# Optimization experiments

Measured on AMD Instinct MI355X. Metric: run time of the kernel, lower is better.

The kernel has to match this reference:

```python
import jax, jax.numpy as jnp
import numpy as np
from jax import lax

K = 7  # kernel_size
PAD = K // 2


def _feature_difference(t):
    # t: [B, C, H, W] -> normalized census-style local differences [B, K*K, H, W]
    intensity = t.mean(axis=1, keepdims=True)  # [B,1,H,W]
    # Equivalent to conv2d with the identity (eye) kernel in the torch module:
    # channel k gathers the neighbor at offset (k//K, k%K) with zero padding.
    patches = lax.conv_general_dilated_patches(
        intensity, filter_shape=(K, K), window_strides=(1, 1),
        padding=[(PAD, PAD), (PAD, PAD)])  # [B, K*K, H, W]
    local_diff = patches - intensity
    return local_diff / jnp.sqrt(0.81 + local_diff * local_diff)


def setup_inputs() -> dict:
    key = jax.random.key(0)
    kx, ky = jax.random.split(key)
    B, C, H, W = 8, 3, 320, 1024
    x = jax.random.uniform(kx, (B, C, H, W), dtype=jnp.float32)
    y = jax.random.uniform(ky, (B, C, H, W), dtype=jnp.float32)
    return {"x": x, "y": y}


def reference(x, y):
    diff_x = _feature_difference(x)
    diff_y = _feature_difference(y)
    diff_total = diff_x - lax.stop_gradient(diff_y)  # .detach() on y branch
    d2 = diff_total * diff_total
    dist = (d2 / (0.1 + d2)).mean(axis=1, keepdims=True)  # [B,1,H,W]
    b, c, h, w = x.shape
    # valid-region mask: ones in the interior, zeros in the PAD-wide border
    mask = jnp.zeros((b, 1, h, w), dtype=x.dtype)
    mask = mask.at[:, :, PAD:h - PAD, PAD:w - PAD].set(1.0)
    return (dist * mask).mean()
```

## Files before the change

kernel.cpp:

```cpp
#include <hip/hip_runtime.h>

typedef float f32x2 __attribute__((ext_vector_type(2)));
typedef float f32x4 __attribute__((ext_vector_type(4)));

#define PAD 3
#define HH 320
#define WW 1024
#define BB 8
#define TH 32
#define TW 64
#define HALO_H (TH + 2*PAD)
#define LDS_W  72
#define NF4    (LDS_W/4)
#define NPOS   (HALO_H * NF4)
#define RPW 4
#define NWAVES 8
#define NTHREADS (NWAVES * 64)

#define NIN ((HH - 2*PAD) * (WW - 2*PAD))
#define OUT_SCALE (1.0 / (49.0 * (double)BB * (double)HH * (double)WW))
#define C0 ((float)(48.0 * (double)BB * (double)NIN * OUT_SCALE))
#define NEG_SCALE ((float)(-0.1 * OUT_SCALE))

#define KEEP(v) asm("" : "+v"(v))

__device__ __forceinline__ f32x2 mk2(float a, float b) { f32x2 r; r.x = a; r.y = b; return r; }
__device__ __forceinline__ f32x2 sp2(float a)          { f32x2 r; r.x = a; r.y = a; return r; }
__device__ __forceinline__ f32x2 fma2(f32x2 a, f32x2 b, f32x2 c) {
    return __builtin_elementwise_fma(a, b, c);
}

template<bool INTERIOR>
__device__ __forceinline__ void pair2(f32x2 nx, f32x2 ny, f32x2 cx2, f32x2 cy2,
                                      f32x2 w2, float& acc)
{
    f32x2 dx  = nx - cx2;
    f32x2 dy  = ny - cy2;
    f32x2 dx2 = dx * dx;
    f32x2 dy2 = dy * dy;
    f32x2 ax  = dx2 + sp2(0.81f);
    f32x2 ay  = dy2 + sp2(0.81f);
    f32x2 P   = ax * ay;
    f32x2 s   = mk2(__builtin_amdgcn_rsqf(P.x), __builtin_amdgcn_rsqf(P.y));
    f32x2 A   = fma2(dx2, ay, dy2 * ax);
    f32x2 h   = dx * dy;
    f32x2 inner = fma2(s, A, h * sp2(-2.0f));
    f32x2 t2  = s * inner;
    f32x2 den = t2 + sp2(0.1f);
    float ip    = __builtin_amdgcn_rcpf(den.x * den.y);
    float cross;
    if constexpr (INTERIOR) cross = den.x + den.y;
    else                    cross = fmaf(w2.x, den.y, w2.y * den.x);
    acc = fmaf(ip, cross, acc);
}

template<bool INTERIOR>
__device__ __forceinline__ float compute_rows(
    const float (&sIx)[HALO_H][LDS_W], const float (&sIy)[HALO_H][LDS_W],
    int tile_i, int tile_j, int tx, int wv)
{
    float cO[7] = {};
    f32x2 cP0 = {}, cP1 = {}, cP2 = {}, cP3 = {};
    if constexpr (!INTERIOR) {
        const int gj = tile_j + tx;
        #pragma unroll
        for (int d = 0; d < 7; ++d) {
            int nj = gj + d - 3;
            cO[d] = (nj >= PAD && nj < WW - PAD) ? 1.0f : 0.0f;
        }
        cP0 = mk2(cO[0], cO[1]);
        cP1 = mk2(cO[2], cO[3]);
        cP2 = mk2(cO[4], cO[5]);
        cP3 = sp2(cO[6]);
    }

    const int li0 = wv * RPW;

    float wx[4][7], wy[4][7];
    #pragma unroll
    for (int r = 0; r < 3; ++r) {
        #pragma unroll
        for (int d = 0; d < 7; ++d) {
            float a = sIx[li0 + 3 + r][tx + 1 + d]; KEEP(a); wx[r][d] = a;
            float c = sIy[li0 + 3 + r][tx + 1 + d]; KEEP(c); wy[r][d] = c;
        }
    }

    float acc = 0.0f;

    #pragma unroll
    for (int iu = 0; iu < RPW; ++iu) {
        const int li = li0 + iu;
        const int gi = tile_i + li;
        const int snew = (iu + 3) & 3;
        #pragma unroll
        for (int d = 0; d < 7; ++d) {
            float a = sIx[li + 6][tx + 1 + d]; KEEP(a); wx[snew][d] = a;
            float c = sIy[li + 6][tx + 1 + d]; KEEP(c); wy[snew][d] = c;
        }

        float rin[4] = {};
        f32x2 mc2 = {};
        if constexpr (!INTERIOR) {
            #pragma unroll
            for (int di = 0; di < 4; ++di) {
                int ni = gi + di;
                rin[di] = (ni >= PAD && ni < HH - PAD) ? 1.0f : 0.0f;
            }
            mc2 = sp2(rin[0] * cO[3]);
        }

        const int s0 = iu & 3;
        const f32x2 cx2 = sp2(wx[s0][3]);
        const f32x2 cy2 = sp2(wy[s0][3]);

        pair2<INTERIOR>(mk2(wx[s0][4], wx[s0][5]), mk2(wy[s0][4], wy[s0][5]),
              cx2, cy2, INTERIOR ? sp2(0.0f) : fma2(sp2(rin[0]), cP2, mc2), acc);

        #pragma unroll
        for (int di = 1; di <= 3; ++di) {
            const int s = (iu + di) & 3;
            const f32x2 rin2 = sp2(rin[di]);
            pair2<INTERIOR>(mk2(wx[s][0], wx[s][1]), mk2(wy[s][0], wy[s][1]),
                  cx2, cy2, INTERIOR ? sp2(0.0f) : fma2(rin2, cP0, mc2), acc);
            pair2<INTERIOR>(mk2(wx[s][2], wx[s][3]), mk2(wy[s][2], wy[s][3]),
                  cx2, cy2, INTERIOR ? sp2(0.0f) : fma2(rin2, cP1, mc2), acc);
            pair2<INTERIOR>(mk2(wx[s][4], wx[s][5]), mk2(wy[s][4], wy[s][5]),
                  cx2, cy2, INTERIOR ? sp2(0.0f) : fma2(rin2, cP2, mc2), acc);
        }

        {
            const int s1 = (iu + 1) & 3;
            const int s2 = (iu + 2) & 3;
            const int s3 = (iu + 3) & 3;
            pair2<INTERIOR>(mk2(wx[s0][6], wx[s1][6]), mk2(wy[s0][6], wy[s1][6]),
                  cx2, cy2, INTERIOR ? sp2(0.0f) : fma2(mk2(rin[0], rin[1]), cP3, mc2), acc);
            pair2<INTERIOR>(mk2(wx[s2][6], wx[s3][6]), mk2(wy[s2][6], wy[s3][6]),
                  cx2, cy2, INTERIOR ? sp2(0.0f) : fma2(mk2(rin[2], rin[3]), cP3, mc2), acc);
        }
    }

    return acc;
}

__global__ __launch_bounds__(NTHREADS, 4) void ternary_loss_kernel(
    const float* __restrict__ x, const float* __restrict__ y,
    float* __restrict__ out)
{
    __shared__ __align__(16) float sIx[HALO_H][LDS_W];
    __shared__ __align__(16) float sIy[HALO_H][LDS_W];
    __shared__ float wave_sums[NWAVES];

    const int tile_j = blockIdx.x * TW;
    const int tile_i = blockIdx.y * TH;
    const int b      = blockIdx.z;
    const int tx  = threadIdx.x;
    const int wv  = threadIdx.y;
    const int tid = wv * 64 + tx;

    const size_t PLANE = (size_t)HH * WW;
    const float* xb = x + (size_t)b * 3 * PLANE;
    const float* yb = y + (size_t)b * 3 * PLANE;

    for (int p = tid; p < NPOS; p += NTHREADS) {
        int r  = p / NF4;
        int c4 = p - r * NF4;
        int gi  = tile_i - PAD + r;
        int gj0 = tile_j - 4 + 4 * c4;
        f32x4 vx = {0.0f, 0.0f, 0.0f, 0.0f};
        f32x4 vy = {0.0f, 0.0f, 0.0f, 0.0f};
        if ((unsigned)gi < (unsigned)HH && (unsigned)gj0 < (unsigned)WW) {
            const float* px = xb + (size_t)gi * WW + gj0;
            f32x4 a0 = *(const f32x4*)(px);
            f32x4 a1 = *(const f32x4*)(px + PLANE);
            f32x4 a2 = *(const f32x4*)(px + 2 * PLANE);
            vx = (a0 + a1 + a2) * (1.0f / 3.0f);
            const float* py = yb + (size_t)gi * WW + gj0;
            f32x4 b0 = *(const f32x4*)(py);
            f32x4 b1 = *(const f32x4*)(py + PLANE);
            f32x4 b2 = *(const f32x4*)(py + 2 * PLANE);
            vy = (b0 + b1 + b2) * (1.0f / 3.0f);
        }
        *(f32x4*)&sIx[r][4 * c4] = vx;
        *(f32x4*)&sIy[r][4 * c4] = vy;
    }
    __syncthreads();

    const bool interior = (tile_i >= PAD) && (tile_i + TH + PAD <= HH - PAD)
                       && (tile_j >= 2*PAD) && (tile_j + TW + PAD <= WW - PAD);

    float acc;
    if (interior) acc = 2.0f * compute_rows<true >(sIx, sIy, tile_i, tile_j, tx, wv);
    else          acc =        compute_rows<false>(sIx, sIy, tile_i, tile_j, tx, wv);

    #pragma unroll
    for (int off = 32; off > 0; off >>= 1)
        acc += __shfl_down(acc, off, 64);
    if (tx == 0) wave_sums[wv] = acc;
    __syncthreads();
    if (tid == 0) {
        float total = 0.0f;
        #pragma unroll
        for (int w = 0; w < NWAVES; ++w) total += wave_sums[w];
        total *= NEG_SCALE;
        if (blockIdx.x == 0 && blockIdx.y == 0 && blockIdx.z == 0)
            total += C0;
        atomicAdd(out, total);
    }
}

extern "C" void kernel_launch(void* const* d_in, const int* in_sizes, int n_in,
                              void* d_out, int out_size, void* d_ws, size_t ws_size,
                              hipStream_t stream) {
    const float* x = (const float*)d_in[0];
    const float* y = (const float*)d_in[1];
    float* out = (float*)d_out;

    hipMemsetAsync(out, 0, sizeof(float), stream);

    dim3 grid(WW / TW, HH / TH, BB);
    dim3 block(64, NWAVES, 1);
    ternary_loss_kernel<<<grid, block, 0, stream>>>(x, y, out);
}
```

Before: 115.9 us.

## Use explicit packed f32 inline asm, halve waves per block, double rows per wave

Rewrites the pairwise math with hand-written v_pk_add/mul/fma_f32 inline assembly so the compiler cannot split the packed operations into scalar ones, and hoists the constants into registers that are passed in. The sliding window is now held as packed f32x2 pairs. Blocks go from 8 waves of 4 rows to 4 waves of 8 rows, with an outer loop that is not unrolled, so each block has fewer threads and more work per thread. Inline asm hides the instructions from the scheduler and may force extra moves or hurt latency hiding, and fewer waves per block lowers the parallelism available within each block.

```diff
diff --git a/kernel.cpp b/kernel.cpp
--- a/kernel.cpp
+++ b/kernel.cpp
@@ -13,8 +13,8 @@
 #define LDS_W  72
 #define NF4    (LDS_W/4)
 #define NPOS   (HALO_H * NF4)
-#define RPW 4
-#define NWAVES 8
+#define RPW 8
+#define NWAVES 4
 #define NTHREADS (NWAVES * 64)
 
 #define NIN ((HH - 2*PAD) * (WW - 2*PAD))
@@ -22,46 +22,63 @@
 #define C0 ((float)(48.0 * (double)BB * (double)NIN * OUT_SCALE))
 #define NEG_SCALE ((float)(-0.1 * OUT_SCALE))
 
-#define KEEP(v) asm("" : "+v"(v))
-
-__device__ __forceinline__ f32x2 mk2(float a, float b) { f32x2 r; r.x = a; r.y = b; return r; }
-__device__ __forceinline__ f32x2 sp2(float a)          { f32x2 r; r.x = a; r.y = a; return r; }
-__device__ __forceinline__ f32x2 fma2(f32x2 a, f32x2 b, f32x2 c) {
-    return __builtin_elementwise_fma(a, b, c);
-}
+#define KEEP2(v) asm("" : "+v"(v))
+
+static __device__ __forceinline__ f32x2 mk2(float a, float b){ f32x2 r; r.x=a; r.y=b; return r; }
+static __device__ __forceinline__ f32x2 sp2(float a){ f32x2 r; r.x=a; r.y=a; return r; }
+
+static __device__ __forceinline__ f32x2 pk_add(f32x2 a, f32x2 b){
+    f32x2 d; asm("v_pk_add_f32 %0, %1, %2" : "=v"(d) : "v"(a), "v"(b)); return d; }
+static __device__ __forceinline__ f32x2 pk_mul(f32x2 a, f32x2 b){
+    f32x2 d; asm("v_pk_mul_f32 %0, %1, %2" : "=v"(d) : "v"(a), "v"(b)); return d; }
+static __device__ __forceinline__ f32x2 pk_fma(f32x2 a, f32x2 b, f32x2 c){
+    f32x2 d; asm("v_pk_fma_f32 %0, %1, %2, %3" : "=v"(d) : "v"(a), "v"(b), "v"(c)); return d; }
 
 template<bool INTERIOR>
-__device__ __forceinline__ void pair2(f32x2 nx, f32x2 ny, f32x2 cx2, f32x2 cy2,
-                                      f32x2 w2, float& acc)
+static __device__ __forceinline__ void pair2(f32x2 nx, f32x2 ny,
+    f32x2 mcx2, f32x2 mcy2, f32x2 c081, f32x2 cm2, f32x2 c01,
+    f32x2 w2, float& acc)
 {
-    f32x2 dx  = nx - cx2;
-    f32x2 dy  = ny - cy2;
-    f32x2 dx2 = dx * dx;
-    f32x2 dy2 = dy * dy;
-    f32x2 ax  = dx2 + sp2(0.81f);
-    f32x2 ay  = dy2 + sp2(0.81f);
-    f32x2 P   = ax * ay;
-    f32x2 s   = mk2(__builtin_amdgcn_rsqf(P.x), __builtin_amdgcn_rsqf(P.y));
-    f32x2 A   = fma2(dx2, ay, dy2 * ax);
-    f32x2 h   = dx * dy;
-    f32x2 inner = fma2(s, A, h * sp2(-2.0f));
-    f32x2 t2  = s * inner;
-    f32x2 den = t2 + sp2(0.1f);
-    float ip    = __builtin_amdgcn_rcpf(den.x * den.y);
+    f32x2 dx  = pk_add(nx, mcx2);
+    f32x2 dy  = pk_add(ny, mcy2);
+    f32x2 dx2 = pk_mul(dx, dx);
+    f32x2 dy2 = pk_mul(dy, dy);
+    f32x2 ax  = pk_add(dx2, c081);
+    f32x2 ay  = pk_add(dy2, c081);
+    f32x2 P   = pk_mul(ax, ay);
+    f32x2 s; s.x = __builtin_amdgcn_rsqf(P.x); s.y = __builtin_amdgcn_rsqf(P.y);
+    f32x2 A   = pk_fma(dx2, ay, pk_mul(dy2, ax));
+    f32x2 hm  = pk_mul(pk_mul(dx, dy), cm2);
+    f32x2 t2  = pk_mul(s, pk_fma(s, A, hm));
+    f32x2 den = pk_add(t2, c01);
+    float ip  = __builtin_amdgcn_rcpf(den.x * den.y);
     float cross;
     if constexpr (INTERIOR) cross = den.x + den.y;
     else                    cross = fmaf(w2.x, den.y, w2.y * den.x);
     acc = fmaf(ip, cross, acc);
 }
 
+#define LOADROW(ARR, ROW, P, S) do {                         \
+    P[0].x = ARR[ROW][tx+1]; P[0].y = ARR[ROW][tx+2];        \
+    P[1].x = ARR[ROW][tx+3]; P[1].y = ARR[ROW][tx+4];        \
+    P[2].x = ARR[ROW][tx+5]; P[2].y = ARR[ROW][tx+6];        \
+    S      = ARR[ROW][tx+7];                                 \
+    KEEP2(P[0]); KEEP2(P[1]); KEEP2(P[2]);                   \
+} while (0)
+
 template<bool INTERIOR>
-__device__ __forceinline__ float compute_rows(
+static __device__ __forceinline__ float compute_rows(
     const float (&sIx)[HALO_H][LDS_W], const float (&sIy)[HALO_H][LDS_W],
     int tile_i, int tile_j, int tx, int wv)
 {
-    float cO[7] = {};
+    const f32x2 c081 = sp2(0.81f);
+    const f32x2 cm2  = sp2(-2.0f);
+    const f32x2 c01  = sp2(0.1f);
+
+    float cO3 = 0.0f;
     f32x2 cP0 = {}, cP1 = {}, cP2 = {}, cP3 = {};
     if constexpr (!INTERIOR) {
+        float cO[7];
         const int gj = tile_j + tx;
         #pragma unroll
         for (int d = 0; d < 7; ++d) {
@@ -72,71 +89,69 @@
         cP1 = mk2(cO[2], cO[3]);
         cP2 = mk2(cO[4], cO[5]);
         cP3 = sp2(cO[6]);
+        cO3 = cO[3];
     }
 
     const int li0 = wv * RPW;
 
-    float wx[4][7], wy[4][7];
+    f32x2 px[4][3], py[4][3];
+    float sx6[4], sy6[4];
     #pragma unroll
     for (int r = 0; r < 3; ++r) {
+        LOADROW(sIx, li0 + 3 + r, px[r], sx6[r]);
+        LOADROW(sIy, li0 + 3 + r, py[r], sy6[r]);
+    }
+
+    float acc = 0.0f;
+
+    #pragma unroll 1
+    for (int io = 0; io < RPW / 4; ++io) {
         #pragma unroll
-        for (int d = 0; d < 7; ++d) {
-            float a = sIx[li0 + 3 + r][tx + 1 + d]; KEEP(a); wx[r][d] = a;
-            float c = sIy[li0 + 3 + r][tx + 1 + d]; KEEP(c); wy[r][d] = c;
-        }
-    }
-
-    float acc = 0.0f;
-
-    #pragma unroll
-    for (int iu = 0; iu < RPW; ++iu) {
-        const int li = li0 + iu;
-        const int gi = tile_i + li;
-        const int snew = (iu + 3) & 3;
-        #pragma unroll
-        for (int d = 0; d < 7; ++d) {
-            float a = sIx[li + 6][tx + 1 + d]; KEEP(a); wx[snew][d] = a;
-            float c = sIy[li + 6][tx + 1 + d]; KEEP(c); wy[snew][d] = c;
-        }
-
-        float rin[4] = {};
-        f32x2 mc2 = {};
-        if constexpr (!INTERIOR) {
+        for (int iu = 0; iu < 4; ++iu) {
+            const int li = li0 + io * 4 + iu;
+            const int gi = tile_i + li;
+            const int sn = (iu + 3) & 3;
+            LOADROW(sIx, li + 6, px[sn], sx6[sn]);
+            LOADROW(sIy, li + 6, py[sn], sy6[sn]);
+
+            float rin[4] = {};
+            f32x2 mc2 = {};
+            if constexpr (!INTERIOR) {
+                #pragma unroll
+                for (int di = 0; di < 4; ++di) {
+                    int ni = gi + di;
+                    rin[di] = (ni >= PAD && ni < HH - PAD) ? 1.0f : 0.0f;
+                }
+                mc2 = sp2(rin[0] * cO3);
+            }
+
+            const int s0 = iu & 3, s1 = (iu+1)&3, s2 = (iu+2)&3, s3 = (iu+3)&3;
+            const float cx = px[s0][1].y;
+            const float cy = py[s0][1].y;
+            const f32x2 mcx2 = sp2(-cx);
+            const f32x2 mcy2 = sp2(-cy);
+
+            pair2<INTERIOR>(px[s0][2], py[s0][2], mcx2, mcy2, c081, cm2, c01,
+                INTERIOR ? c01 : pk_fma(sp2(rin[0]), cP2, mc2), acc);
+
             #pragma unroll
-            for (int di = 0; di < 4; ++di) {
-                int ni = gi + di;
-                rin[di] = (ni >= PAD && ni < HH - PAD) ? 1.0f : 0.0f;
+            for (int di = 1; di <= 3; ++di) {
+                const int s = (iu + di) & 3;
+                const f32x2 rin2 = sp2(rin[di]);
+                pair2<INTERIOR>(px[s][0], py[s][0], mcx2, mcy2, c081, cm2, c01,
+                    INTERIOR ? c01 : pk_fma(rin2, cP0, mc2), acc);
+                pair2<INTERIOR>(px[s][1], py[s][1], mcx2, mcy2, c081, cm2, c01,
+                    INTERIOR ? c01 : pk_fma(rin2, cP1, mc2), acc);
+                pair2<INTERIOR>(px[s][2], py[s][2], mcx2, mcy2, c081, cm2, c01,
+                    INTERIOR ? c01 : pk_fma(rin2, cP2, mc2), acc);
             }
-            mc2 = sp2(rin[0] * cO[3]);
-        }
-
-        const int s0 = iu & 3;
-        const f32x2 cx2 = sp2(wx[s0][3]);
-        const f32x2 cy2 = sp2(wy[s0][3]);
-
-        pair2<INTERIOR>(mk2(wx[s0][4], wx[s0][5]), mk2(wy[s0][4], wy[s0][5]),
-              cx2, cy2, INTERIOR ? sp2(0.0f) : fma2(sp2(rin[0]), cP2, mc2), acc);
-
-        #pragma unroll
-        for (int di = 1; di <= 3; ++di) {
-            const int s = (iu + di) & 3;
-            const f32x2 rin2 = sp2(rin[di]);
-            pair2<INTERIOR>(mk2(wx[s][0], wx[s][1]), mk2(wy[s][0], wy[s][1]),
-                  cx2, cy2, INTERIOR ? sp2(0.0f) : fma2(rin2, cP0, mc2), acc);
-            pair2<INTERIOR>(mk2(wx[s][2], wx[s][3]), mk2(wy[s][2], wy[s][3]),
-                  cx2, cy2, INTERIOR ? sp2(0.0f) : fma2(rin2, cP1, mc2), acc);
-            pair2<INTERIOR>(mk2(wx[s][4], wx[s][5]), mk2(wy[s][4], wy[s][5]),
-                  cx2, cy2, INTERIOR ? sp2(0.0f) : fma2(rin2, cP2, mc2), acc);
-        }
-
-        {
-            const int s1 = (iu + 1) & 3;
-            const int s2 = (iu + 2) & 3;
-            const int s3 = (iu + 3) & 3;
-            pair2<INTERIOR>(mk2(wx[s0][6], wx[s1][6]), mk2(wy[s0][6], wy[s1][6]),
-                  cx2, cy2, INTERIOR ? sp2(0.0f) : fma2(mk2(rin[0], rin[1]), cP3, mc2), acc);
-            pair2<INTERIOR>(mk2(wx[s2][6], wx[s3][6]), mk2(wy[s2][6], wy[s3][6]),
-                  cx2, cy2, INTERIOR ? sp2(0.0f) : fma2(mk2(rin[2], rin[3]), cP3, mc2), acc);
+
+            pair2<INTERIOR>(mk2(sx6[s0], sx6[s1]), mk2(sy6[s0], sy6[s1]),
+                mcx2, mcy2, c081, cm2, c01,
+                INTERIOR ? c01 : pk_fma(mk2(rin[0], rin[1]), cP3, mc2), acc);
+            pair2<INTERIOR>(mk2(sx6[s2], sx6[s3]), mk2(sy6[s2], sy6[s3]),
+                mcx2, mcy2, c081, cm2, c01,
+                INTERIOR ? c01 : pk_fma(mk2(rin[2], rin[3]), cP3, mc2), acc);
         }
     }
 
@@ -199,10 +214,7 @@
     if (tx == 0) wave_sums[wv] = acc;
     __syncthreads();
     if (tid == 0) {
-        float total = 0.0f;
-        #pragma unroll
-        for (int w = 0; w < NWAVES; ++w) total += wave_sums[w];
-        total *= NEG_SCALE;
+        float total = (wave_sums[0] + wave_sums[1] + wave_sums[2] + wave_sums[3]) * NEG_SCALE;
         if (blockIdx.x == 0 && blockIdx.y == 0 && blockIdx.z == 0)
             total += C0;
         atomicAdd(out, total);
```

Result: slower. 119.9 us (+3.4%).

## Replace LDS halo tiles with per-lane strips and ds_bpermute neighbor exchange

Applied to the files above, without the earlier changes.

Drops the shared-memory staging of channel-mean tiles. Each lane now owns one column and walks a 10-row strip, loading its rows directly from global memory with software prefetch. Horizontal neighbors come from cross-lane ds_bpermute, with overlapping 58-column wave tiles and masking of the edge lanes. This removes the LDS fill and the __syncthreads before compute, but adds bpermute traffic, redundant halo computation in 6 of every 64 lanes, and scalar (non-vector) global loads.

```diff
diff --git a/kernel.cpp b/kernel.cpp
--- a/kernel.cpp
+++ b/kernel.cpp
@@ -1,38 +1,38 @@
 #include <hip/hip_runtime.h>
 
 typedef float f32x2 __attribute__((ext_vector_type(2)));
-typedef float f32x4 __attribute__((ext_vector_type(4)));
 
 #define PAD 3
 #define HH 320
 #define WW 1024
 #define BB 8
-#define TH 32
-#define TW 64
-#define HALO_H (TH + 2*PAD)
-#define LDS_W  72
-#define NF4    (LDS_W/4)
-#define NPOS   (HALO_H * NF4)
-#define RPW 4
-#define NWAVES 8
-#define NTHREADS (NWAVES * 64)
+#define PLANE ((size_t)HH * WW)
+
+#define TWO 58
+#define NCT 18
+#define TH 40
+#define NRT 8
+#define RPW 10
+#define NWAVES 4
+#define NTHREADS 256
 
 #define NIN ((HH - 2*PAD) * (WW - 2*PAD))
 #define OUT_SCALE (1.0 / (49.0 * (double)BB * (double)HH * (double)WW))
 #define C0 ((float)(48.0 * (double)BB * (double)NIN * OUT_SCALE))
 #define NEG_SCALE ((float)(-0.1 * OUT_SCALE))
 
-#define KEEP(v) asm("" : "+v"(v))
-
-__device__ __forceinline__ f32x2 mk2(float a, float b) { f32x2 r; r.x = a; r.y = b; return r; }
-__device__ __forceinline__ f32x2 sp2(float a)          { f32x2 r; r.x = a; r.y = a; return r; }
-__device__ __forceinline__ f32x2 fma2(f32x2 a, f32x2 b, f32x2 c) {
+static __device__ __forceinline__ f32x2 mk2(float a, float b){ f32x2 r; r.x=a; r.y=b; return r; }
+static __device__ __forceinline__ f32x2 sp2(float a){ f32x2 r; r.x=a; r.y=a; return r; }
+static __device__ __forceinline__ f32x2 fma2(f32x2 a, f32x2 b, f32x2 c){
     return __builtin_elementwise_fma(a, b, c);
 }
+static __device__ __forceinline__ float lane_get(float v, int addr){
+    return __int_as_float(__builtin_amdgcn_ds_bpermute(addr, __float_as_int(v)));
+}
 
 template<bool INTERIOR>
-__device__ __forceinline__ void pair2(f32x2 nx, f32x2 ny, f32x2 cx2, f32x2 cy2,
-                                      f32x2 w2, float& acc)
+static __device__ __forceinline__ void pair2(f32x2 nx, f32x2 ny, f32x2 cx2, f32x2 cy2,
+                                             f32x2 w2, float& acc)
 {
     f32x2 dx  = nx - cx2;
     f32x2 dy  = ny - cy2;
@@ -41,13 +41,13 @@
     f32x2 ax  = dx2 + sp2(0.81f);
     f32x2 ay  = dy2 + sp2(0.81f);
     f32x2 P   = ax * ay;
-    f32x2 s   = mk2(__builtin_amdgcn_rsqf(P.x), __builtin_amdgcn_rsqf(P.y));
+    f32x2 s; s.x = __builtin_amdgcn_rsqf(P.x); s.y = __builtin_amdgcn_rsqf(P.y);
     f32x2 A   = fma2(dx2, ay, dy2 * ax);
     f32x2 h   = dx * dy;
     f32x2 inner = fma2(s, A, h * sp2(-2.0f));
     f32x2 t2  = s * inner;
     f32x2 den = t2 + sp2(0.1f);
-    float ip    = __builtin_amdgcn_rcpf(den.x * den.y);
+    float ip  = __builtin_amdgcn_rcpf(den.x * den.y);
     float cross;
     if constexpr (INTERIOR) cross = den.x + den.y;
     else                    cross = fmaf(w2.x, den.y, w2.y * den.x);
@@ -55,50 +55,65 @@
 }
 
 template<bool INTERIOR>
-__device__ __forceinline__ float compute_rows(
-    const float (&sIx)[HALO_H][LDS_W], const float (&sIy)[HALO_H][LDS_W],
-    int tile_i, int tile_j, int tx, int wv)
+static __device__ __forceinline__ float strip(
+    const float* __restrict__ xb, const float* __restrict__ yb,
+    int gi0, int colJ, float colF3,
+    int adm3, int adm2, int adm1, int adp1, int adp2, int adp3)
 {
-    float cO[7] = {};
+    float cO3 = 0.0f;
     f32x2 cP0 = {}, cP1 = {}, cP2 = {}, cP3 = {};
     if constexpr (!INTERIOR) {
-        const int gj = tile_j + tx;
+        float cO[7];
         #pragma unroll
         for (int d = 0; d < 7; ++d) {
-            int nj = gj + d - 3;
+            int nj = colJ + d - 3;
             cO[d] = (nj >= PAD && nj < WW - PAD) ? 1.0f : 0.0f;
         }
         cP0 = mk2(cO[0], cO[1]);
         cP1 = mk2(cO[2], cO[3]);
         cP2 = mk2(cO[4], cO[5]);
         cP3 = sp2(cO[6]);
+        cO3 = cO[3];
     }
 
-    const int li0 = wv * RPW;
-
+    float Lx[3][3], Ly[3][3], s3r[3];
     float wx[4][7], wy[4][7];
-    #pragma unroll
-    for (int r = 0; r < 3; ++r) {
-        #pragma unroll
-        for (int d = 0; d < 7; ++d) {
-            float a = sIx[li0 + 3 + r][tx + 1 + d]; KEEP(a); wx[r][d] = a;
-            float c = sIy[li0 + 3 + r][tx + 1 + d]; KEEP(c); wy[r][d] = c;
-        }
-    }
+
+#define ISSUE(r) { \
+    const int ri_ = (r) % 3; \
+    const int gr_ = gi0 + (r); \
+    const int gc_ = (gr_ < HH) ? gr_ : (HH - 1); \
+    const float* bx_ = xb + (size_t)gc_ * WW; \
+    const float* by_ = yb + (size_t)gc_ * WW; \
+    Lx[ri_][0] = bx_[0]; Lx[ri_][1] = bx_[PLANE]; Lx[ri_][2] = bx_[2*PLANE]; \
+    Ly[ri_][0] = by_[0]; Ly[ri_][1] = by_[PLANE]; Ly[ri_][2] = by_[2*PLANE]; \
+    s3r[ri_] = (gr_ < HH) ? colF3 : 0.0f; }
+
+#define PROC(r, SL) { \
+    const int ri_ = (r) % 3; \
+    const float Ix_ = (Lx[ri_][0] + Lx[ri_][1] + Lx[ri_][2]) * s3r[ri_]; \
+    const float Iy_ = (Ly[ri_][0] + Ly[ri_][1] + Ly[ri_][2]) * s3r[ri_]; \
+    wx[SL][3] = Ix_;                    wy[SL][3] = Iy_; \
+    wx[SL][0] = lane_get(Ix_, adm3);    wy[SL][0] = lane_get(Iy_, adm3); \
+    wx[SL][1] = lane_get(Ix_, adm2);    wy[SL][1] = lane_get(Iy_, adm2); \
+    wx[SL][2] = lane_get(Ix_, adm1);    wy[SL][2] = lane_get(Iy_, adm1); \
+    wx[SL][4] = lane_get(Ix_, adp1);    wy[SL][4] = lane_get(Iy_, adp1); \
+    wx[SL][5] = lane_get(Ix_, adp2);    wy[SL][5] = lane_get(Iy_, adp2); \
+    wx[SL][6] = lane_get(Ix_, adp3);    wy[SL][6] = lane_get(Iy_, adp3); }
+
+    ISSUE(0) ISSUE(1) ISSUE(2)
+    PROC(0, 0) ISSUE(3)
+    PROC(1, 1) ISSUE(4)
+    PROC(2, 2)
 
     float acc = 0.0f;
 
     #pragma unroll
     for (int iu = 0; iu < RPW; ++iu) {
-        const int li = li0 + iu;
-        const int gi = tile_i + li;
-        const int snew = (iu + 3) & 3;
-        #pragma unroll
-        for (int d = 0; d < 7; ++d) {
-            float a = sIx[li + 6][tx + 1 + d]; KEEP(a); wx[snew][d] = a;
-            float c = sIy[li + 6][tx + 1 + d]; KEEP(c); wy[snew][d] = c;
-        }
-
+        if (iu + 5 <= RPW + 2) ISSUE(iu + 5)
+        PROC(iu + 3, ((iu + 3) & 3))
+
+        const int gi = gi0 + iu;
         float rin[4] = {};
         f32x2 mc2 = {};
         if constexpr (!INTERIOR) {
@@ -107,39 +122,35 @@
                 int ni = gi + di;
                 rin[di] = (ni >= PAD && ni < HH - PAD) ? 1.0f : 0.0f;
             }
-            mc2 = sp2(rin[0] * cO[3]);
+            mc2 = sp2(rin[0] * cO3);
         }
 
-        const int s0 = iu & 3;
+        const int s0 = iu & 3, s1 = (iu+1)&3, s2 = (iu+2)&3, s3_ = (iu+3)&3;
         const f32x2 cx2 = sp2(wx[s0][3]);
         const f32x2 cy2 = sp2(wy[s0][3]);
 
         pair2<INTERIOR>(mk2(wx[s0][4], wx[s0][5]), mk2(wy[s0][4], wy[s0][5]),
-              cx2, cy2, INTERIOR ? sp2(0.0f) : fma2(sp2(rin[0]), cP2, mc2), acc);
+            cx2, cy2, INTERIOR ? sp2(0.0f) : fma2(sp2(rin[0]), cP2, mc2), acc);
 
         #pragma unroll
         for (int di = 1; di <= 3; ++di) {
             const int s = (iu + di) & 3;
             const f32x2 rin2 = sp2(rin[di]);
             pair2<INTERIOR>(mk2(wx[s][0], wx[s][1]), mk2(wy[s][0], wy[s][1]),
-                  cx2, cy2, INTERIOR ? sp2(0.0f) : fma2(rin2, cP0, mc2), acc);
+                cx2, cy2, INTERIOR ? sp2(0.0f) : fma2(rin2, cP0, mc2), acc);
             pair2<INTERIOR>(mk2(wx[s][2], wx[s][3]), mk2(wy[s][2], wy[s][3]),
-                  cx2, cy2, INTERIOR ? sp2(0.0f) : fma2(rin2, cP1, mc2), acc);
+                cx2, cy2, INTERIOR ? sp2(0.0f) : fma2(rin2, cP1, mc2), acc);
             pair2<INTERIOR>(mk2(wx[s][4], wx[s][5]), mk2(wy[s][4], wy[s][5]),
-                  cx2, cy2, INTERIOR ? sp2(0.0f) : fma2(rin2, cP2, mc2), acc);
+                cx2, cy2, INTERIOR ? sp2(0.0f) : fma2(rin2, cP2, mc2), acc);
         }
 
-        {
-            const int s1 = (iu + 1) & 3;
-            const int s2 = (iu + 2) & 3;
-            const int s3 = (iu + 3) & 3;
-            pair2<INTERIOR>(mk2(wx[s0][6], wx[s1][6]), mk2(wy[s0][6], wy[s1][6]),
-                  cx2, cy2, INTERIOR ? sp2(0.0f) : fma2(mk2(rin[0], rin[1]), cP3, mc2), acc);
-            pair2<INTERIOR>(mk2(wx[s2][6], wx[s3][6]), mk2(wy[s2][6], wy[s3][6]),
-                  cx2, cy2, INTERIOR ? sp2(0.0f) : fma2(mk2(rin[2], rin[3]), cP3, mc2), acc);
-        }
+        pair2<INTERIOR>(mk2(wx[s0][6], wx[s1][6]), mk2(wy[s0][6], wy[s1][6]),
+            cx2, cy2, INTERIOR ? sp2(0.0f) : fma2(mk2(rin[0], rin[1]), cP3, mc2), acc);
+        pair2<INTERIOR>(mk2(wx[s2][6], wx[s3_][6]), mk2(wy[s2][6], wy[s3_][6]),
+            cx2, cy2, INTERIOR ? sp2(0.0f) : fma2(mk2(rin[2], rin[3]), cP3, mc2), acc);
     }
-
+#undef ISSUE
+#undef PROC
     return acc;
 }
 
@@ -147,51 +158,43 @@
     const float* __restrict__ x, const float* __restrict__ y,
     float* __restrict__ out)
 {
-    __shared__ __align__(16) float sIx[HALO_H][LDS_W];
-    __shared__ __align__(16) float sIy[HALO_H][LDS_W];
     __shared__ float wave_sums[NWAVES];
 
-    const int tile_j = blockIdx.x * TW;
+    const int t      = blockIdx.x;
     const int tile_i = blockIdx.y * TH;
     const int b      = blockIdx.z;
     const int tx  = threadIdx.x;
     const int wv  = threadIdx.y;
     const int tid = wv * 64 + tx;
 
-    const size_t PLANE = (size_t)HH * WW;
-    const float* xb = x + (size_t)b * 3 * PLANE;
-    const float* yb = y + (size_t)b * 3 * PLANE;
-
-    for (int p = tid; p < NPOS; p += NTHREADS) {
-        int r  = p / NF4;
-        int c4 = p - r * NF4;
-        int gi  = tile_i - PAD + r;
-        int gj0 = tile_j - 4 + 4 * c4;
-        f32x4 vx = {0.0f, 0.0f, 0.0f, 0.0f};
-        f32x4 vy = {0.0f, 0.0f, 0.0f, 0.0f};
-        if ((unsigned)gi < (unsigned)HH && (unsigned)gj0 < (unsigned)WW) {
-            const float* px = xb + (size_t)gi * WW + gj0;
-            f32x4 a0 = *(const f32x4*)(px);
-            f32x4 a1 = *(const f32x4*)(px + PLANE);
-            f32x4 a2 = *(const f32x4*)(px + 2 * PLANE);
-            vx = (a0 + a1 + a2) * (1.0f / 3.0f);
-            const float* py = yb + (size_t)gi * WW + gj0;
-            f32x4 b0 = *(const f32x4*)(py);
-            f32x4 b1 = *(const f32x4*)(py + PLANE);
-            f32x4 b2 = *(const f32x4*)(py + 2 * PLANE);
-            vy = (b0 + b1 + b2) * (1.0f / 3.0f);
-        }
-        *(f32x4*)&sIx[r][4 * c4] = vx;
-        *(f32x4*)&sIy[r][4 * c4] = vy;
-    }
-    __syncthreads();
-
-    const bool interior = (tile_i >= PAD) && (tile_i + TH + PAD <= HH - PAD)
-                       && (tile_j >= 2*PAD) && (tile_j + TW + PAD <= WW - PAD);
+    const int colJ   = t * TWO + tx;
+    const int colC   = (colJ < WW) ? colJ : (WW - 1);
+    const float colF3 = (colJ < WW) ? (1.0f / 3.0f) : 0.0f;
+
+    const float* xb = x + (size_t)b * 3 * PLANE + colC;
+    const float* yb = y + (size_t)b * 3 * PLANE + colC;
+    const int gi0 = tile_i + wv * RPW;
+
+    const int adm3 = ((tx - 3) & 63) << 2;
+    const int adm2 = ((tx - 2) & 63) << 2;
+    const int adm1 = ((tx - 1) & 63) << 2;
+    const int adp1 = ((tx + 1) & 63) << 2;
+    const int adp2 = ((tx + 2) & 63) << 2;
+    const int adp3 = ((tx + 3) & 63) << 2;
+
+    const float activeF = ((tx <= 60) && (tx >= 3 || t == 0)) ? 1.0f : 0.0f;
+
+    const bool interior = (t >= 1) && (t <= NCT - 2)
+                       && (tile_i >= PAD) && (tile_i + TH - 1 + PAD <= HH - PAD - 1);
 
     float acc;
-    if (interior) acc = 2.0f * compute_rows<true >(sIx, sIy, tile_i, tile_j, tx, wv);
-    else          acc =        compute_rows<false>(sIx, sIy, tile_i, tile_j, tx, wv);
+    if (interior)
+        acc = 2.0f * strip<true >(xb, yb, gi0, colJ, colF3,
+                                  adm3, adm2, adm1, adp1, adp2, adp3);
+    else
+        acc =        strip<false>(xb, yb, gi0, colJ, colF3,
+                                  adm3, adm2, adm1, adp1, adp2, adp3);
+    acc *= activeF;
 
     #pragma unroll
     for (int off = 32; off > 0; off >>= 1)
@@ -199,10 +202,7 @@
     if (tx == 0) wave_sums[wv] = acc;
     __syncthreads();
     if (tid == 0) {
-        float total = 0.0f;
-        #pragma unroll
-        for (int w = 0; w < NWAVES; ++w) total += wave_sums[w];
-        total *= NEG_SCALE;
+        float total = (wave_sums[0] + wave_sums[1] + wave_sums[2] + wave_sums[3]) * NEG_SCALE;
         if (blockIdx.x == 0 && blockIdx.y == 0 && blockIdx.z == 0)
             total += C0;
         atomicAdd(out, total);
@@ -218,7 +218,7 @@
 
     hipMemsetAsync(out, 0, sizeof(float), stream);
 
-    dim3 grid(WW / TW, HH / TH, BB);
+    dim3 grid(NCT, NRT, BB);
     dim3 block(64, NWAVES, 1);
     ternary_loss_kernel<<<grid, block, 0, stream>>>(x, y, out);
 }
```

Measured after the change: 267.0 us. 2.3x slower.

## Halve waves per block and overlap second-half halo load with first-half compute

Applied to the files above, without the earlier changes.

Cuts the block from 8 waves to 4, so each wave now processes 8 rows in two halves of 4. The first 22 halo rows are staged into LDS up front, and the global loads for the remaining rows are issued into registers before the first half's compute, then written to LDS afterwards. This is meant to hide global-memory latency behind compute and reduce per-block staging stalls. In exchange there is an extra barrier, more register pressure from the in-flight loads, and fewer threads sharing the staging work. Loads for out-of-range halo positions are redirected to offset 0 and masked to zero.

```diff
diff --git a/kernel.cpp b/kernel.cpp
--- a/kernel.cpp
+++ b/kernel.cpp
@@ -12,10 +12,11 @@
 #define HALO_H (TH + 2*PAD)
 #define LDS_W  72
 #define NF4    (LDS_W/4)
-#define NPOS   (HALO_H * NF4)
-#define RPW 4
-#define NWAVES 8
-#define NTHREADS (NWAVES * 64)
+#define NWAVES 4
+#define NTHREADS 256
+#define ROWS_A 22
+#define NPOS_A (ROWS_A * NF4)
+#define NPOS_B ((HALO_H - ROWS_A) * NF4)
 
 #define NIN ((HH - 2*PAD) * (WW - 2*PAD))
 #define OUT_SCALE (1.0 / (49.0 * (double)BB * (double)HH * (double)WW))
@@ -24,15 +25,15 @@
 
 #define KEEP(v) asm("" : "+v"(v))
 
-__device__ __forceinline__ f32x2 mk2(float a, float b) { f32x2 r; r.x = a; r.y = b; return r; }
-__device__ __forceinline__ f32x2 sp2(float a)          { f32x2 r; r.x = a; r.y = a; return r; }
-__device__ __forceinline__ f32x2 fma2(f32x2 a, f32x2 b, f32x2 c) {
+static __device__ __forceinline__ f32x2 mk2(float a, float b){ f32x2 r; r.x=a; r.y=b; return r; }
+static __device__ __forceinline__ f32x2 sp2(float a){ f32x2 r; r.x=a; r.y=a; return r; }
+static __device__ __forceinline__ f32x2 fma2(f32x2 a, f32x2 b, f32x2 c){
     return __builtin_elementwise_fma(a, b, c);
 }
 
 template<bool INTERIOR>
-__device__ __forceinline__ void pair2(f32x2 nx, f32x2 ny, f32x2 cx2, f32x2 cy2,
-                                      f32x2 w2, float& acc)
+static __device__ __forceinline__ void pair2(f32x2 nx, f32x2 ny, f32x2 cx2, f32x2 cy2,
+                                             f32x2 w2, float& acc)
 {
     f32x2 dx  = nx - cx2;
     f32x2 dy  = ny - cy2;
@@ -41,27 +42,54 @@
     f32x2 ax  = dx2 + sp2(0.81f);
     f32x2 ay  = dy2 + sp2(0.81f);
     f32x2 P   = ax * ay;
-    f32x2 s   = mk2(__builtin_amdgcn_rsqf(P.x), __builtin_amdgcn_rsqf(P.y));
+    f32x2 s; s.x = __builtin_amdgcn_rsqf(P.x); s.y = __builtin_amdgcn_rsqf(P.y);
     f32x2 A   = fma2(dx2, ay, dy2 * ax);
     f32x2 h   = dx * dy;
     f32x2 inner = fma2(s, A, h * sp2(-2.0f));
     f32x2 t2  = s * inner;
     f32x2 den = t2 + sp2(0.1f);
-    float ip    = __builtin_amdgcn_rcpf(den.x * den.y);
+    float ip  = __builtin_amdgcn_rcpf(den.x * den.y);
     float cross;
     if constexpr (INTERIOR) cross = den.x + den.y;
     else                    cross = fmaf(w2.x, den.y, w2.y * den.x);
     acc = fmaf(ip, cross, acc);
 }
 
+static __device__ __forceinline__ void stage_pos(
+    float (&sIx)[HALO_H][LDS_W], float (&sIy)[HALO_H][LDS_W],
+    const float* __restrict__ xb, const float* __restrict__ yb,
+    int tile_i, int tile_j, int r, int c4)
+{
+    const size_t PLANE = (size_t)HH * WW;
+    int gi  = tile_i - PAD + r;
+    int gj0 = tile_j - 4 + 4 * c4;
+    f32x4 vx = {0.0f, 0.0f, 0.0f, 0.0f};
+    f32x4 vy = {0.0f, 0.0f, 0.0f, 0.0f};
+    if ((unsigned)gi < (unsigned)HH && (unsigned)gj0 < (unsigned)WW) {
+        const float* px = xb + (size_t)gi * WW + gj0;
+        f32x4 a0 = *(const f32x4*)(px);
+        f32x4 a1 = *(const f32x4*)(px + PLANE);
+        f32x4 a2 = *(const f32x4*)(px + 2 * PLANE);
+        vx = (a0 + a1 + a2) * (1.0f / 3.0f);
+        const float* py = yb + (size_t)gi * WW + gj0;
+        f32x4 b0 = *(const f32x4*)(py);
+        f32x4 b1 = *(const f32x4*)(py + PLANE);
+        f32x4 b2 = *(const f32x4*)(py + 2 * PLANE);
+        vy = (b0 + b1 + b2) * (1.0f / 3.0f);
+    }
+    *(f32x4*)&sIx[r][4 * c4] = vx;
+    *(f32x4*)&sIy[r][4 * c4] = vy;
+}
+
 template<bool INTERIOR>
-__device__ __forceinline__ float compute_rows(
+static __device__ __forceinline__ float compute_half(
     const float (&sIx)[HALO_H][LDS_W], const float (&sIy)[HALO_H][LDS_W],
-    int tile_i, int tile_j, int tx, int wv)
-{
-    float cO[7] = {};
+    int tile_i, int tile_j, int tx, int wv, int li_base)
+{
+    float cO3 = 0.0f;
     f32x2 cP0 = {}, cP1 = {}, cP2 = {}, cP3 = {};
     if constexpr (!INTERIOR) {
+        float cO[7];
         const int gj = tile_j + tx;
         #pragma unroll
         for (int d = 0; d < 7; ++d) {
@@ -72,9 +100,10 @@
         cP1 = mk2(cO[2], cO[3]);
         cP2 = mk2(cO[4], cO[5]);
         cP3 = sp2(cO[6]);
-    }
-
-    const int li0 = wv * RPW;
+        cO3 = cO[3];
+    }
+
+    const int li0 = li_base + wv * 4;
 
     float wx[4][7], wy[4][7];
     #pragma unroll
@@ -89,14 +118,14 @@
     float acc = 0.0f;
 
     #pragma unroll
-    for (int iu = 0; iu < RPW; ++iu) {
+    for (int iu = 0; iu < 4; ++iu) {
         const int li = li0 + iu;
         const int gi = tile_i + li;
-        const int snew = (iu + 3) & 3;
+        const int sn = (iu + 3) & 3;
         #pragma unroll
         for (int d = 0; d < 7; ++d) {
-            float a = sIx[li + 6][tx + 1 + d]; KEEP(a); wx[snew][d] = a;
-            float c = sIy[li + 6][tx + 1 + d]; KEEP(c); wy[snew][d] = c;
+            float a = sIx[li + 6][tx + 1 + d]; KEEP(a); wx[sn][d] = a;
+            float c = sIy[li + 6][tx + 1 + d]; KEEP(c); wy[sn][d] = c;
         }
 
         float rin[4] = {};
@@ -107,37 +136,32 @@
                 int ni = gi + di;
                 rin[di] = (ni >= PAD && ni < HH - PAD) ? 1.0f : 0.0f;
             }
-            mc2 = sp2(rin[0] * cO[3]);
-        }
-
-        const int s0 = iu & 3;
+            mc2 = sp2(rin[0] * cO3);
+        }
+
+        const int s0 = iu & 3, s1 = (iu+1)&3, s2 = (iu+2)&3, s3_ = (iu+3)&3;
         const f32x2 cx2 = sp2(wx[s0][3]);
         const f32x2 cy2 = sp2(wy[s0][3]);
 
         pair2<INTERIOR>(mk2(wx[s0][4], wx[s0][5]), mk2(wy[s0][4], wy[s0][5]),
-              cx2, cy2, INTERIOR ? sp2(0.0f) : fma2(sp2(rin[0]), cP2, mc2), acc);
+            cx2, cy2, INTERIOR ? sp2(0.0f) : fma2(sp2(rin[0]), cP2, mc2), acc);
 
         #pragma unroll
         for (int di = 1; di <= 3; ++di) {
             const int s = (iu + di) & 3;
             const f32x2 rin2 = sp2(rin[di]);
             pair2<INTERIOR>(mk2(wx[s][0], wx[s][1]), mk2(wy[s][0], wy[s][1]),
-                  cx2, cy2, INTERIOR ? sp2(0.0f) : fma2(rin2, cP0, mc2), acc);
+                cx2, cy2, INTERIOR ? sp2(0.0f) : fma2(rin2, cP0, mc2), acc);
             pair2<INTERIOR>(mk2(wx[s][2], wx[s][3]), mk2(wy[s][2], wy[s][3]),
-                  cx2, cy2, INTERIOR ? sp2(0.0f) : fma2(rin2, cP1, mc2), acc);
+                cx2, cy2, INTERIOR ? sp2(0.0f) : fma2(rin2, cP1, mc2), acc);
             pair2<INTERIOR>(mk2(wx[s][4], wx[s][5]), mk2(wy[s][4], wy[s][5]),
-                  cx2, cy2, INTERIOR ? sp2(0.0f) : fma2(rin2, cP2, mc2), acc);
-        }
-
-        {
-            const int s1 = (iu + 1) & 3;
-            const int s2 = (iu + 2) & 3;
-            const int s3 = (iu + 3) & 3;
-            pair2<INTERIOR>(mk2(wx[s0][6], wx[s1][6]), mk2(wy[s0][6], wy[s1][6]),
-                  cx2, cy2, INTERIOR ? sp2(0.0f) : fma2(mk2(rin[0], rin[1]), cP3, mc2), acc);
-            pair2<INTERIOR>(mk2(wx[s2][6], wx[s3][6]), mk2(wy[s2][6], wy[s3][6]),
-                  cx2, cy2, INTERIOR ? sp2(0.0f) : fma2(mk2(rin[2], rin[3]), cP3, mc2), acc);
-        }
+                cx2, cy2, INTERIOR ? sp2(0.0f) : fma2(rin2, cP2, mc2), acc);
+        }
+
+        pair2<INTERIOR>(mk2(wx[s0][6], wx[s1][6]), mk2(wy[s0][6], wy[s1][6]),
+            cx2, cy2, INTERIOR ? sp2(0.0f) : fma2(mk2(rin[0], rin[1]), cP3, mc2), acc);
+        pair2<INTERIOR>(mk2(wx[s2][6], wx[s3_][6]), mk2(wy[s2][6], wy[s3_][6]),
+            cx2, cy2, INTERIOR ? sp2(0.0f) : fma2(mk2(rin[2], rin[3]), cP3, mc2), acc);
     }
 
     return acc;
@@ -162,36 +186,54 @@
     const float* xb = x + (size_t)b * 3 * PLANE;
     const float* yb = y + (size_t)b * 3 * PLANE;
 
-    for (int p = tid; p < NPOS; p += NTHREADS) {
+    for (int p = tid; p < NPOS_A; p += NTHREADS) {
         int r  = p / NF4;
         int c4 = p - r * NF4;
-        int gi  = tile_i - PAD + r;
-        int gj0 = tile_j - 4 + 4 * c4;
-        f32x4 vx = {0.0f, 0.0f, 0.0f, 0.0f};
-        f32x4 vy = {0.0f, 0.0f, 0.0f, 0.0f};
-        if ((unsigned)gi < (unsigned)HH && (unsigned)gj0 < (unsigned)WW) {
-            const float* px = xb + (size_t)gi * WW + gj0;
-            f32x4 a0 = *(const f32x4*)(px);
-            f32x4 a1 = *(const f32x4*)(px + PLANE);
-            f32x4 a2 = *(const f32x4*)(px + 2 * PLANE);
-            vx = (a0 + a1 + a2) * (1.0f / 3.0f);
-            const float* py = yb + (size_t)gi * WW + gj0;
-            f32x4 b0 = *(const f32x4*)(py);
-            f32x4 b1 = *(const f32x4*)(py + PLANE);
-            f32x4 b2 = *(const f32x4*)(py + 2 * PLANE);
-            vy = (b0 + b1 + b2) * (1.0f / 3.0f);
-        }
-        *(f32x4*)&sIx[r][4 * c4] = vx;
-        *(f32x4*)&sIy[r][4 * c4] = vy;
+        stage_pos(sIx, sIy, xb, yb, tile_i, tile_j, r, c4);
     }
     __syncthreads();
+
+    const int rB  = ROWS_A + tid / NF4;
+    const int cB  = tid - (tid / NF4) * NF4;
+    const int giB = tile_i - PAD + rB;
+    const int gjB = tile_j - 4 + 4 * cB;
+    const bool okB = ((unsigned)giB < (unsigned)HH) && ((unsigned)gjB < (unsigned)WW);
+    const size_t offB = okB ? ((size_t)giB * WW + gjB) : 0;
+    const float* pxB = xb + offB;
+    const float* pyB = yb + offB;
+    f32x4 bx0 = *(const f32x4*)(pxB);
+    f32x4 bx1 = *(const f32x4*)(pxB + PLANE);
+    f32x4 bx2 = *(const f32x4*)(pxB + 2 * PLANE);
+    f32x4 by0 = *(const f32x4*)(pyB);
+    f32x4 by1 = *(const f32x4*)(pyB + PLANE);
+    f32x4 by2 = *(const f32x4*)(pyB + 2 * PLANE);
+    const float mB = okB ? (1.0f / 3.0f) : 0.0f;
 
     const bool interior = (tile_i >= PAD) && (tile_i + TH + PAD <= HH - PAD)
                        && (tile_j >= 2*PAD) && (tile_j + TW + PAD <= WW - PAD);
 
     float acc;
-    if (interior) acc = 2.0f * compute_rows<true >(sIx, sIy, tile_i, tile_j, tx, wv);
-    else          acc =        compute_rows<false>(sIx, sIy, tile_i, tile_j, tx, wv);
+    if (interior) acc = compute_half<true >(sIx, sIy, tile_i, tile_j, tx, wv, 0);
+    else          acc = compute_half<false>(sIx, sIy, tile_i, tile_j, tx, wv, 0);
+
+    {
+        f32x4 vx = (bx0 + bx1 + bx2) * mB;
+        f32x4 vy = (by0 + by1 + by2) * mB;
+        *(f32x4*)&sIx[rB][4 * cB] = vx;
+        *(f32x4*)&sIy[rB][4 * cB] = vy;
+    }
+    if (tid < NPOS_B - NTHREADS) {
+        int q  = NTHREADS + tid;
+        int r  = ROWS_A + q / NF4;
+        int c4 = q - (q / NF4) * NF4;
+        stage_pos(sIx, sIy, xb, yb, tile_i, tile_j, r, c4);
+    }
+    __syncthreads();
+
+    if (interior) acc += compute_half<true >(sIx, sIy, tile_i, tile_j, tx, wv, 16);
+    else          acc += compute_half<false>(sIx, sIy, tile_i, tile_j, tx, wv, 16);
+
+    if (interior) acc *= 2.0f;
 
     #pragma unroll
     for (int off = 32; off > 0; off >>= 1)
@@ -199,10 +241,7 @@
     if (tx == 0) wave_sums[wv] = acc;
     __syncthreads();
     if (tid == 0) {
-        float total = 0.0f;
-        #pragma unroll
-        for (int w = 0; w < NWAVES; ++w) total += wave_sums[w];
-        total *= NEG_SCALE;
+        float total = (wave_sums[0] + wave_sums[1] + wave_sums[2] + wave_sums[3]) * NEG_SCALE;
         if (blockIdx.x == 0 && blockIdx.y == 0 && blockIdx.z == 0)
             total += C0;
         atomicAdd(out, total);
```

Result: no change. 118.2 us (+1.9%).
